# Optimization experiments

Hardware: AMD Instinct MI355X
Metric: run time of the kernel (lower is better)

Reference implementation:

```python
import jax, jax.numpy as jnp
import numpy as np

PAIR_KEY_BASE = 20000  # token_max + 1
POS_WEIGHT = 1.0
NEG_WEIGHT = 1.0
EPS = 1e-8


def _isin_sorted(x, sorted_keys):
    # torch.isin equivalent given a sorted 1-D key set
    idx = jnp.searchsorted(sorted_keys, x)
    idx = jnp.clip(idx, 0, sorted_keys.shape[0] - 1)
    return sorted_keys[idx] == x


def setup_inputs() -> dict:
    key = jax.random.key(0)
    k_ids, k_tf, k_act, k_prior, k_u, k_v = jax.random.split(key, 6)
    B, S, D, M = 8, 2048, 64, 200000
    input_ids = jax.random.randint(k_ids, (B, S), 0, PAIR_KEY_BASE, dtype=jnp.int32)
    tf_mask = jax.random.randint(k_tf, (B, S), 0, 2) == 1
    active_gene_mask = jax.random.randint(k_act, (B, S), 0, 2) == 1
    # prior GRN pair keys: src*base + tgt, sorted (duplicates are harmless for isin)
    prior_pair_keys = jnp.sort(jax.random.randint(
        k_prior, (M,), 0, PAIR_KEY_BASE * PAIR_KEY_BASE, dtype=jnp.int32))
    # u, v small positive so u @ v^T lands mostly inside (0, 1) before clamping
    u = jax.random.uniform(k_u, (B, S, D), dtype=jnp.float32) * 0.1
    v = jax.random.uniform(k_v, (B, S, D), dtype=jnp.float32) * 0.1
    return {"input_ids": input_ids, "tf_mask": tf_mask,
            "active_gene_mask": active_gene_mask,
            "prior_pair_keys": prior_pair_keys, "u": u, "v": v}


def reference(input_ids, tf_mask, active_gene_mask, prior_pair_keys, u, v):
    # supervise: TF rows x active-gene cols  [B,S,S]
    supervise = tf_mask[:, :, None] & active_gene_mask[:, None, :]
    # pair keys for every (src, tgt) position pair  [B,S,S]
    pair_keys = input_ids[:, :, None] * PAIR_KEY_BASE + input_ids[:, None, :]
    positive = _isin_sorted(pair_keys, prior_pair_keys) & supervise
    target = positive.astype(jnp.float32)
    # edge probabilities, clamped like torch: [B,S,S]
    edge_prob = jnp.clip(jnp.einsum('bsd,btd->bst', u, v), EPS, 1.0 - EPS)
    # binary cross entropy, reduction='none'
    loss = -(target * jnp.log(edge_prob) + (1.0 - target) * jnp.log1p(-edge_prob))
    weight = target * POS_WEIGHT + (1.0 - target) * NEG_WEIGHT
    # neg_sample_ratio=None -> sampled_mask == supervise_mask
    m = supervise.astype(jnp.float32)
    numer = jnp.sum(loss * weight * m)
    denom = jnp.sum(weight * m)
    return numer / (denom + EPS)
```

## Files before the change

### kernel.cpp

```cpp
#include <hip/hip_runtime.h>
#include <math.h>

#define BB 8
#define SS 2048
#define DD 64
#define PAIR_BASE 20000
#define CEPS 1e-8f
#define NROWS (BB * SS)
#define MAIN_BLOCKS (16 * 16 * BB)
#define PPMAX 1024
#define PREP_BLOCKS (64 + BB + BB + 1)

typedef __bf16 bf16x8 __attribute__((ext_vector_type(8)));
typedef __bf16 bf16x4 __attribute__((ext_vector_type(4)));
typedef float  f32x4  __attribute__((ext_vector_type(4)));

struct Ws {
    int byteMode;
    int pad;
    int mc[BB];
    int nc[BB];
    float mpart[MAIN_BLOCKS];
    float ppart[PPMAX];
    int cheadR[BB * PAIR_BASE];
    int cnextR[NROWS];
    int cheadC[BB * PAIR_BASE];
    int cnextC[NROWS];
    __bf16 Uc[(size_t)BB * SS * DD];
    __bf16 Vc[(size_t)BB * SS * DD];
};

__device__ __forceinline__ bool read_mask(const void* p, int i, int byteMode) {
    if (byteMode) return ((const unsigned char*)p)[i] != 0;
    return ((const int*)p)[i] != 0;
}

__device__ __forceinline__ int detect_bm(const void* tf_raw, int tid, int* badl) {
    if (tid == 0) *badl = 0;
    __syncthreads();
    if (((const unsigned int*)tf_raw)[tid] > 1u) atomicOr(badl, 1);
    __syncthreads();
    return *badl;
}

__global__ __launch_bounds__(1024) void prep_kernel(
    const int* __restrict__ ids,
    const void* __restrict__ tf_raw,
    const void* __restrict__ act_raw,
    const float* __restrict__ u,
    const float* __restrict__ v,
    Ws* __restrict__ ws)
{
    __shared__ int badl;
    __shared__ int wsum[16], wbase[16], stot;
    __shared__ unsigned short cidx[SS];

    const int blk  = blockIdx.x;
    const int tid  = threadIdx.x;
    const int w    = tid >> 6;
    const int lane = tid & 63;

    if (blk < 64) {
        const int b     = blk >> 3;
        const int slice = blk & 7;
        const int bm = detect_bm(tf_raw, tid, &badl);
        const unsigned long long below = ((unsigned long long)1 << lane) - 1;

        for (int phase = 0; phase < 2; ++phase) {
            const void* mraw = phase ? act_raw : tf_raw;
            const int e0 = b * SS + 2 * tid;
            const int m0 = read_mask(mraw, e0,     bm) ? 1 : 0;
            const int m1 = read_mask(mraw, e0 + 1, bm) ? 1 : 0;
            const unsigned long long k0 = __ballot(m0 != 0);
            const unsigned long long k1 = __ballot(m1 != 0);
            const int exclw = __popcll(k0 & below) + __popcll(k1 & below);
            if (lane == 0) wsum[w] = __popcll(k0) + __popcll(k1);
            __syncthreads();
            if (tid == 0) {
                int run = 0;
                #pragma unroll
                for (int k = 0; k < 16; ++k) { wbase[k] = run; run += wsum[k]; }
                stot = run;
            }
            __syncthreads();
            const int excl = wbase[w] + exclw;
            if (m0) cidx[excl]      = (unsigned short)(2 * tid);
            if (m1) cidx[excl + m0] = (unsigned short)(2 * tid + 1);
            __syncthreads();
            const int total = stot;
            if (tid == 0 && slice == 0) {
                if (phase) ws->nc[b] = total; else ws->mc[b] = total;
            }
            const int tpad = (total + 127) & ~127;
            const int rbeg = slice * 256;
            const int rend = min(rbeg + 256, tpad);
            __bf16* dst = (phase ? ws->Vc : ws->Uc) + (size_t)b * SS * DD;
            const float* src = (phase ? v : u) + (size_t)b * SS * DD;
            const int r_off = tid >> 4, c = tid & 15;
            #pragma unroll
            for (int p4 = 0; p4 < 4; ++p4) {
                const int r = rbeg + p4 * 64 + r_off;
                if (r < rend) {
                    bf16x4 hv;
                    if (r < total) {
                        const float4 f = *(const float4*)(src + (size_t)cidx[r] * DD + c * 4);
                        hv = (bf16x4){ (__bf16)f.x, (__bf16)f.y, (__bf16)f.z, (__bf16)f.w };
                    } else {
                        hv = (bf16x4){ (__bf16)0.f, (__bf16)0.f, (__bf16)0.f, (__bf16)0.f };
                    }
                    *(bf16x4*)(dst + (size_t)r * DD + c * 4) = hv;
                }
            }
            __syncthreads();
        }
    } else if (blk < 64 + BB) {
        const int b = blk - 64;
        const int bm = detect_bm(tf_raw, tid, &badl);
        int* head = ws->cheadR + b * PAIR_BASE;
        for (int i = tid; i < PAIR_BASE; i += 1024) head[i] = -1;
        __syncthreads();
        for (int s = tid; s < SS; s += 1024) {
            if (read_mask(tf_raw, b * SS + s, bm)) {
                const int id = ids[b * SS + s];
                const int old = atomicExch(&head[id], s);
                ws->cnextR[b * SS + s] = old;
            }
        }
    } else if (blk < 64 + 2 * BB) {
        const int b = blk - (64 + BB);
        const int bm = detect_bm(tf_raw, tid, &badl);
        int* head = ws->cheadC + b * PAIR_BASE;
        for (int i = tid; i < PAIR_BASE; i += 1024) head[i] = -1;
        __syncthreads();
        for (int t = tid; t < SS; t += 1024) {
            if (read_mask(act_raw, b * SS + t, bm)) {
                const int id = ids[b * SS + t];
                const int old = atomicExch(&head[id], t);
                ws->cnextC[b * SS + t] = old;
            }
        }
    } else {
        const int bm = detect_bm(tf_raw, tid, &badl);
        if (tid == 0) ws->byteMode = bm;
    }
}

__global__ __launch_bounds__(256) void work_kernel(
    const int* __restrict__ prior, int M,
    const float* __restrict__ u,
    const float* __restrict__ v,
    Ws* __restrict__ ws)
{
    __shared__ __align__(16) __bf16 Ulds[128 * 72];
    __shared__ __align__(16) __bf16 Vlds[128 * 72];
    __shared__ float wsumS[4];

    const int bid  = blockIdx.x;
    const int tid  = threadIdx.x;
    const int w    = tid >> 6;
    const int lane = tid & 63;

    float lsum = 0.f;
    float* slot;

    if (bid < MAIN_BLOCKS) {
        const int b  = bid >> 8;
        const int by = (bid >> 4) & 15;
        const int bx = bid & 15;
        const int s0 = by * 128;
        const int t0 = bx * 128;
        slot = &ws->mpart[bid];

        const int mcp = (ws->mc[b] + 127) & ~127;
        const int ncp = (ws->nc[b] + 127) & ~127;
        if (s0 < mcp && t0 < ncp) {
            const __bf16* ub = ws->Uc + (size_t)(b * SS + s0) * DD;
            const __bf16* vb = ws->Vc + (size_t)(b * SS + t0) * DD;
            #pragma unroll
            for (int it = 0; it < 4; ++it) {
                int li = tid + it * 256;
                int r  = li >> 3;
                int c8 = li & 7;
                *(bf16x8*)&Ulds[r * 72 + c8 * 8] = *(const bf16x8*)(ub + r * DD + c8 * 8);
                *(bf16x8*)&Vlds[r * 72 + c8 * 8] = *(const bf16x8*)(vb + r * DD + c8 * 8);
            }
            __syncthreads();

            const int quad = lane >> 4;
            const int l15  = lane & 15;
            const int wm0  = (w >> 1) * 64;
            const int wn0  = (w & 1) * 64;

            f32x4 acc[4][4];
            #pragma unroll
            for (int i = 0; i < 4; ++i)
                #pragma unroll
                for (int j = 0; j < 4; ++j)
                    acc[i][j] = (f32x4){0.f, 0.f, 0.f, 0.f};

            #pragma unroll
            for (int kh = 0; kh < 2; ++kh) {
                const int kcol = kh * 32 + quad * 8;
                bf16x8 af[4], bfr[4];
                #pragma unroll
                for (int ti = 0; ti < 4; ++ti)
                    af[ti] = *(const bf16x8*)&Ulds[(wm0 + ti * 16 + l15) * 72 + kcol];
                #pragma unroll
                for (int tj = 0; tj < 4; ++tj)
                    bfr[tj] = *(const bf16x8*)&Vlds[(wn0 + tj * 16 + l15) * 72 + kcol];
                #pragma unroll
                for (int ti = 0; ti < 4; ++ti)
                    #pragma unroll
                    for (int tj = 0; tj < 4; ++tj)
                        acc[ti][tj] = __builtin_amdgcn_mfma_f32_16x16x32_bf16(
                            af[ti], bfr[tj], acc[ti][tj], 0, 0, 0);
            }

            #pragma unroll
            for (int ti = 0; ti < 4; ++ti)
                #pragma unroll
                for (int r = 0; r < 4; ++r)
                    #pragma unroll
                    for (int tj = 0; tj < 4; ++tj) {
                        float q = 1.0f - acc[ti][tj][r];
                        q = fminf(fmaxf(q, CEPS), 1.0f - CEPS);
                        lsum += __logf(q);
                    }
            lsum = -lsum;
        }
    } else {
        const int pid = bid - MAIN_BLOCKS;
        const int i   = pid * 256 + tid;
        slot = &ws->ppart[pid];

        if (i < M) {
            const int key = prior[i];
            const bool dup = (i > 0) && (prior[i - 1] == key);
            if (!dup) {
                const unsigned int uk  = (unsigned int)key;
                const unsigned int src = uk / PAIR_BASE;
                const unsigned int tgt = uk - src * PAIR_BASE;
                #pragma unroll
                for (int b = 0; b < BB; ++b) {
                    int r = ws->cheadR[b * PAIR_BASE + (int)src];
                    if (r < 0) continue;
                    const int thead = ws->cheadC[b * PAIR_BASE + (int)tgt];
                    if (thead < 0) continue;
                    const int* nxtR = ws->cnextR + b * SS;
                    const int* nxtC = ws->cnextC + b * SS;
                    for (; r >= 0; r = nxtR[r]) {
                        const float* urow = u + (size_t)(b * SS + r) * DD;
                        for (int t = thead; t >= 0; t = nxtC[t]) {
                            const float* vrow = v + (size_t)(b * SS + t) * DD;
                            float dot = 0.f;
                            #pragma unroll
                            for (int k2 = 0; k2 < DD; k2 += 4) {
                                float4 a = *(const float4*)(urow + k2);
                                float4 c = *(const float4*)(vrow + k2);
                                dot += (float)(__bf16)a.x * (float)(__bf16)c.x;
                                dot += (float)(__bf16)a.y * (float)(__bf16)c.y;
                                dot += (float)(__bf16)a.z * (float)(__bf16)c.z;
                                dot += (float)(__bf16)a.w * (float)(__bf16)c.w;
                            }
                            float p = fminf(fmaxf(dot, CEPS), 1.0f - CEPS);
                            float q = fminf(fmaxf(1.0f - dot, CEPS), 1.0f - CEPS);
                            lsum += __logf(q) - __logf(p);
                        }
                    }
                }
            }
        }
    }

    #pragma unroll
    for (int o = 32; o > 0; o >>= 1)
        lsum += __shfl_down(lsum, o, 64);
    if (lane == 0) wsumS[w] = lsum;
    __syncthreads();
    if (tid == 0)
        *slot = wsumS[0] + wsumS[1] + wsumS[2] + wsumS[3];
}

__global__ __launch_bounds__(256) void finalize_kernel(const Ws* __restrict__ ws,
                                                       int npp,
                                                       float* __restrict__ out) {
    __shared__ double sred[256];
    const int tid = threadIdx.x;
    double s = 0.0;
    for (int i = tid; i < MAIN_BLOCKS; i += 256) s += (double)ws->mpart[i];
    for (int i = tid; i < npp;         i += 256) s += (double)ws->ppart[i];
    sred[tid] = s;
    __syncthreads();
    for (int o = 128; o > 0; o >>= 1) {
        if (tid < o) sred[tid] += sred[tid + o];
        __syncthreads();
    }
    if (tid == 0) {
        double denom = 0.0;
        for (int b = 0; b < BB; ++b)
            denom += (double)ws->mc[b] * (double)ws->nc[b];
        out[0] = (float)(sred[0] / (denom + 1e-8));
    }
}

extern "C" void kernel_launch(void* const* d_in, const int* in_sizes, int n_in,
                              void* d_out, int out_size, void* d_ws, size_t ws_size,
                              hipStream_t stream) {
    (void)n_in; (void)out_size; (void)ws_size;
    const int*   ids   = (const int*)d_in[0];
    const void*  tf    = d_in[1];
    const void*  act   = d_in[2];
    const int*   prior = (const int*)d_in[3];
    const int    M     = in_sizes[3];
    const float* u     = (const float*)d_in[4];
    const float* v     = (const float*)d_in[5];
    Ws* ws = (Ws*)d_ws;
    float* out = (float*)d_out;

    int npos = (M + 255) / 256;
    if (npos > PPMAX) npos = PPMAX;

    prep_kernel<<<PREP_BLOCKS, 1024, 0, stream>>>(ids, tf, act, u, v, ws);
    work_kernel<<<MAIN_BLOCKS + npos, 256, 0, stream>>>(prior, M, u, v, ws);
    finalize_kernel<<<1, 256, 0, stream>>>(ws, npos, out);
}
```

Before: 115.0 us.

## Gather u/v rows directly in work kernel instead of staging compacted bf16 copies

Result: slower. 124.1 us (+7.9%).

```diff
diff --git a/kernel.cpp b/kernel.cpp
--- a/kernel.cpp
+++ b/kernel.cpp
@@ -9,7 +9,7 @@
 #define NROWS (BB * SS)
 #define MAIN_BLOCKS (16 * 16 * BB)
 #define PPMAX 1024
-#define PREP_BLOCKS (64 + BB + BB + 1)
+#define PREP_BLOCKS (BB + BB + BB + 1)
 
 typedef __bf16 bf16x8 __attribute__((ext_vector_type(8)));
 typedef __bf16 bf16x4 __attribute__((ext_vector_type(4)));
@@ -22,12 +22,12 @@
     int nc[BB];
     float mpart[MAIN_BLOCKS];
     float ppart[PPMAX];
+    unsigned short cidxR[NROWS];
+    unsigned short cidxC[NROWS];
     int cheadR[BB * PAIR_BASE];
     int cnextR[NROWS];
     int cheadC[BB * PAIR_BASE];
     int cnextC[NROWS];
-    __bf16 Uc[(size_t)BB * SS * DD];
-    __bf16 Vc[(size_t)BB * SS * DD];
 };
 
 __device__ __forceinline__ bool read_mask(const void* p, int i, int byteMode) {
@@ -47,27 +47,24 @@
     const int* __restrict__ ids,
     const void* __restrict__ tf_raw,
     const void* __restrict__ act_raw,
-    const float* __restrict__ u,
-    const float* __restrict__ v,
     Ws* __restrict__ ws)
 {
     __shared__ int badl;
     __shared__ int wsum[16], wbase[16], stot;
-    __shared__ unsigned short cidx[SS];
 
     const int blk  = blockIdx.x;
     const int tid  = threadIdx.x;
     const int w    = tid >> 6;
     const int lane = tid & 63;
 
-    if (blk < 64) {
-        const int b     = blk >> 3;
-        const int slice = blk & 7;
+    if (blk < BB) {
+        const int b = blk;
         const int bm = detect_bm(tf_raw, tid, &badl);
         const unsigned long long below = ((unsigned long long)1 << lane) - 1;
 
         for (int phase = 0; phase < 2; ++phase) {
             const void* mraw = phase ? act_raw : tf_raw;
+            unsigned short* cidx = (phase ? ws->cidxC : ws->cidxR) + b * SS;
             const int e0 = b * SS + 2 * tid;
             const int m0 = read_mask(mraw, e0,     bm) ? 1 : 0;
             const int m1 = read_mask(mraw, e0 + 1, bm) ? 1 : 0;
@@ -86,35 +83,13 @@
             const int excl = wbase[w] + exclw;
             if (m0) cidx[excl]      = (unsigned short)(2 * tid);
             if (m1) cidx[excl + m0] = (unsigned short)(2 * tid + 1);
-            __syncthreads();
             const int total = stot;
-            if (tid == 0 && slice == 0) {
-                if (phase) ws->nc[b] = total; else ws->mc[b] = total;
-            }
-            const int tpad = (total + 127) & ~127;
-            const int rbeg = slice * 256;
-            const int rend = min(rbeg + 256, tpad);
-            __bf16* dst = (phase ? ws->Vc : ws->Uc) + (size_t)b * SS * DD;
-            const float* src = (phase ? v : u) + (size_t)b * SS * DD;
-            const int r_off = tid >> 4, c = tid & 15;
-            #pragma unroll
-            for (int p4 = 0; p4 < 4; ++p4) {
-                const int r = rbeg + p4 * 64 + r_off;
-                if (r < rend) {
-                    bf16x4 hv;
-                    if (r < total) {
-                        const float4 f = *(const float4*)(src + (size_t)cidx[r] * DD + c * 4);
-                        hv = (bf16x4){ (__bf16)f.x, (__bf16)f.y, (__bf16)f.z, (__bf16)f.w };
-                    } else {
-                        hv = (bf16x4){ (__bf16)0.f, (__bf16)0.f, (__bf16)0.f, (__bf16)0.f };
-                    }
-                    *(bf16x4*)(dst + (size_t)r * DD + c * 4) = hv;
-                }
-            }
-            __syncthreads();
-        }
-    } else if (blk < 64 + BB) {
-        const int b = blk - 64;
+            if (tid == 0) { if (phase) ws->nc[b] = total; else ws->mc[b] = total; }
+            for (int i = total + tid; i < SS; i += 1024) cidx[i] = 0;
+            __syncthreads();
+        }
+    } else if (blk < 2 * BB) {
+        const int b = blk - BB;
         const int bm = detect_bm(tf_raw, tid, &badl);
         int* head = ws->cheadR + b * PAIR_BASE;
         for (int i = tid; i < PAIR_BASE; i += 1024) head[i] = -1;
@@ -126,8 +101,8 @@
                 ws->cnextR[b * SS + s] = old;
             }
         }
-    } else if (blk < 64 + 2 * BB) {
-        const int b = blk - (64 + BB);
+    } else if (blk < 3 * BB) {
+        const int b = blk - 2 * BB;
         const int bm = detect_bm(tf_raw, tid, &badl);
         int* head = ws->cheadC + b * PAIR_BASE;
         for (int i = tid; i < PAIR_BASE; i += 1024) head[i] = -1;
@@ -153,6 +128,7 @@
 {
     __shared__ __align__(16) __bf16 Ulds[128 * 72];
     __shared__ __align__(16) __bf16 Vlds[128 * 72];
+    __shared__ unsigned short sRows[128], sCols[128];
     __shared__ float wsumS[4];
 
     const int bid  = blockIdx.x;
@@ -171,18 +147,31 @@
         const int t0 = bx * 128;
         slot = &ws->mpart[bid];
 
-        const int mcp = (ws->mc[b] + 127) & ~127;
-        const int ncp = (ws->nc[b] + 127) & ~127;
+        const int mtot = ws->mc[b];
+        const int ntot = ws->nc[b];
+        const int mcp = (mtot + 127) & ~127;
+        const int ncp = (ntot + 127) & ~127;
         if (s0 < mcp && t0 < ncp) {
-            const __bf16* ub = ws->Uc + (size_t)(b * SS + s0) * DD;
-            const __bf16* vb = ws->Vc + (size_t)(b * SS + t0) * DD;
+            if (tid < 128)       sRows[tid]       = ws->cidxR[b * SS + s0 + tid];
+            else                 sCols[tid - 128] = ws->cidxC[b * SS + t0 + (tid - 128)];
+            __syncthreads();
+
+            const float* ubase = u + (size_t)b * SS * DD;
+            const float* vbase = v + (size_t)b * SS * DD;
+            const float4 z4 = {0.f, 0.f, 0.f, 0.f};
             #pragma unroll
-            for (int it = 0; it < 4; ++it) {
-                int li = tid + it * 256;
-                int r  = li >> 3;
-                int c8 = li & 7;
-                *(bf16x8*)&Ulds[r * 72 + c8 * 8] = *(const bf16x8*)(ub + r * DD + c8 * 8);
-                *(bf16x8*)&Vlds[r * 72 + c8 * 8] = *(const bf16x8*)(vb + r * DD + c8 * 8);
+            for (int it = 0; it < 8; ++it) {
+                const int li = tid + it * 256;
+                const int r  = li >> 4;
+                const int c4 = li & 15;
+                const float4 fu = (s0 + r < mtot)
+                    ? *(const float4*)(ubase + (size_t)sRows[r] * DD + c4 * 4) : z4;
+                const float4 fv = (t0 + r < ntot)
+                    ? *(const float4*)(vbase + (size_t)sCols[r] * DD + c4 * 4) : z4;
+                *(bf16x4*)&Ulds[r * 72 + c4 * 4] =
+                    (bf16x4){ (__bf16)fu.x, (__bf16)fu.y, (__bf16)fu.z, (__bf16)fu.w };
+                *(bf16x4*)&Vlds[r * 72 + c4 * 4] =
+                    (bf16x4){ (__bf16)fv.x, (__bf16)fv.y, (__bf16)fv.z, (__bf16)fv.w };
             }
             __syncthreads();
 
@@ -320,7 +309,7 @@
     int npos = (M + 255) / 256;
     if (npos > PPMAX) npos = PPMAX;
 
-    prep_kernel<<<PREP_BLOCKS, 1024, 0, stream>>>(ids, tf, act, u, v, ws);
+    prep_kernel<<<PREP_BLOCKS, 1024, 0, stream>>>(ids, tf, act, ws);
     work_kernel<<<MAIN_BLOCKS + npos, 256, 0, stream>>>(prior, M, u, v, ws);
     finalize_kernel<<<1, 256, 0, stream>>>(ws, npos, out);
 }
```
